# Optimization experiments

Hardware: AMD Instinct MI355X
Metric: run time of the kernel (lower is better)

## Reference

```python
import jax, jax.numpy as jnp
import numpy as np

B, S, IN_DIM = 8, 4096, 1024
N_SLOTS, SLOT_DIM, N_HEADS, CHUNK, TOP_K = 64, 256, 4, 16, 3
EPS_LN = 1e-5


def setup_inputs() -> dict:
    key = jax.random.key(0)
    ks = jax.random.split(key, 8)
    std = 0.02
    return {
        "x": jax.random.normal(ks[0], (B, S, IN_DIM), jnp.float32),
        "slot_memory": jax.random.normal(ks[1], (1, N_SLOTS, SLOT_DIM), jnp.float32) * std,
        "slot_keys": jax.random.normal(ks[2], (N_SLOTS, SLOT_DIM), jnp.float32) * std,
        "W_in": jax.random.normal(ks[3], (IN_DIM, SLOT_DIM), jnp.float32) / np.sqrt(IN_DIM).astype(np.float32),
        "W_write": jax.random.normal(ks[4], (SLOT_DIM, SLOT_DIM), jnp.float32) / np.sqrt(SLOT_DIM).astype(np.float32),
        "W_gate": jax.random.normal(ks[5], (2 * SLOT_DIM, 1), jnp.float32) / np.sqrt(2 * SLOT_DIM).astype(np.float32),
        "b_gate": jnp.zeros((1,), jnp.float32),
        "W_out": jax.random.normal(ks[6], (SLOT_DIM, IN_DIM), jnp.float32) / np.sqrt(SLOT_DIM).astype(np.float32),
        "ln_in_scale": jnp.ones((IN_DIM,), jnp.float32),
        "ln_in_bias": jnp.zeros((IN_DIM,), jnp.float32),
        "ln_s_scale": jnp.ones((SLOT_DIM,), jnp.float32),
        "ln_s_bias": jnp.zeros((SLOT_DIM,), jnp.float32),
    }


def _layer_norm(x, scale, bias):
    m = jnp.mean(x, axis=-1, keepdims=True)
    v = jnp.mean((x - m) ** 2, axis=-1, keepdims=True)
    return (x - m) * jax.lax.rsqrt(v + EPS_LN) * scale + bias


def _l2norm(x):
    n = jnp.sqrt(jnp.sum(x * x, axis=-1, keepdims=True))
    return x / jnp.maximum(n, 1e-12)  # matches F.normalize eps


def _forward(x, slot_memory, slot_keys, W_in, W_write, W_gate, b_gate, W_out,
             ln_in_scale, ln_in_bias, ln_s_scale, ln_s_bias):
    Bx, Sx, _ = x.shape
    hd = SLOT_DIM // N_HEADS
    slots0 = jnp.broadcast_to(slot_memory, (Bx, N_SLOTS, SLOT_DIM))

    # ---- batched read attention over slots ----
    q = _layer_norm(x, ln_in_scale, ln_in_bias) @ W_in          # (B,S,D)
    qh = q.reshape(Bx, Sx, N_HEADS, hd)
    kh = slots0.reshape(Bx, N_SLOTS, N_HEADS, hd)               # k == v == slots
    scores = jnp.einsum('bshd,bnhd->bhsn', qh, kh) * (hd ** -0.5)
    attn = jax.nn.softmax(scores, axis=-1)                      # (B,H,S,N)
    read = jnp.einsum('bhsn,bnhd->bshd', attn, kh).reshape(Bx, Sx, SLOT_DIM)

    # ---- sequential chunked top-k gather/scatter slot write ----
    key_norms = _l2norm(slot_keys)                              # (N,D)
    b_idx = jnp.arange(Bx)[:, None]

    def chunk_step(slots, chunk):                               # chunk: (B,C,D)
        summary = chunk.mean(axis=1)                            # (B,D)
        match = _l2norm(summary) @ key_norms.T                  # (B,N) cosine sim
        _, top_idx = jax.lax.top_k(match, TOP_K)                # (B,K)
        wv = summary @ W_write                                  # (B,D)
        sel = jnp.take_along_axis(slots, top_idx[:, :, None], axis=1)  # (B,K,D)
        gate = jax.nn.sigmoid(
            jnp.concatenate([sel.mean(axis=1), wv], axis=-1) @ W_gate + b_gate)  # (B,1)
        g = gate[:, None, :]
        new_vals = (1.0 - g) * sel + g * wv[:, None, :]         # (B,K,D)
        return slots.at[b_idx, top_idx].set(new_vals), None

    chunks = read.reshape(Bx, Sx // CHUNK, CHUNK, SLOT_DIM).transpose(1, 0, 2, 3)
    slots_f, _ = jax.lax.scan(chunk_step, slots0, chunks)
    new_slots = _layer_norm(slots_f, ln_s_scale, ln_s_bias)

    out = read @ W_out                                          # dropout is identity in eval
    return out, new_slots


def reference(x, slot_memory, slot_keys, W_in, W_write, W_gate, b_gate, W_out,
              ln_in_scale, ln_in_bias, ln_s_scale, ln_s_bias):
    return _forward(x, slot_memory, slot_keys, W_in, W_write, W_gate, b_gate, W_out,
                    ln_in_scale, ln_in_bias, ln_s_scale, ln_s_bias)
```

## Files before the change

kernel.cpp:

```cpp
#include <hip/hip_runtime.h>

typedef __attribute__((ext_vector_type(8))) short s8v;
typedef __attribute__((ext_vector_type(4))) float f4v;

#define PAD1 88
#define PADG 72

union U8 { unsigned u[4]; s8v s; };

__device__ __forceinline__ unsigned short f2bf(float f) {
  unsigned u = __float_as_uint(f);
  u += 0x7fffu + ((u >> 16) & 1u);
  return (unsigned short)(u >> 16);
}
__device__ __forceinline__ unsigned short f2bfc(float f) {
  return (unsigned short)((__float_as_uint(f) + 0x8000u) >> 16);
}
__device__ __forceinline__ float bf2f(unsigned short h) {
  return __uint_as_float(((unsigned)h) << 16);
}
__device__ __forceinline__ void split2(float x0, float x1, unsigned& hp, unsigned& lp) {
  unsigned t0 = __float_as_uint(x0) + 0x8000u;
  unsigned t1 = __float_as_uint(x1) + 0x8000u;
  float h0 = __uint_as_float(t0 & 0xFFFF0000u);
  float h1 = __uint_as_float(t1 & 0xFFFF0000u);
  float l0 = x0 - h0, l1 = x1 - h1;
  hp = __builtin_amdgcn_perm(t1, t0, 0x07060302u);
  lp = __builtin_amdgcn_perm(__float_as_uint(l1) + 0x8000u,
                             __float_as_uint(l0) + 0x8000u, 0x07060302u);
}
__device__ __forceinline__ unsigned pack2(float a, float b) {
  return __builtin_amdgcn_perm(__float_as_uint(b) + 0x8000u,
                               __float_as_uint(a) + 0x8000u, 0x07060302u);
}
__device__ __forceinline__ f4v vmax4(f4v a, f4v b) {
  f4v r; r[0]=fmaxf(a[0],b[0]); r[1]=fmaxf(a[1],b[1]); r[2]=fmaxf(a[2],b[2]); r[3]=fmaxf(a[3],b[3]); return r;
}
__device__ __forceinline__ f4v shflxor4(f4v v, int m) {
  f4v r; r[0]=__shfl_xor(v[0],m); r[1]=__shfl_xor(v[1],m); r[2]=__shfl_xor(v[2],m); r[3]=__shfl_xor(v[3],m); return r;
}
__device__ __forceinline__ f4v exp4(f4v v) {
  f4v r; r[0]=__expf(v[0]); r[1]=__expf(v[1]); r[2]=__expf(v[2]); r[3]=__expf(v[3]); return r;
}

__global__ void k_prep(const float* __restrict__ W_in, const float* __restrict__ lnis,
                       const float* __restrict__ lnib, const float* __restrict__ W_out,
                       const float* __restrict__ skeys, const float* __restrict__ smem0,
                       const float* __restrict__ wgate,
                       unsigned short* __restrict__ wth, unsigned short* __restrict__ wtl,
                       unsigned short* __restrict__ wot, float* __restrict__ keyn,
                       float* __restrict__ d0, float* __restrict__ uvec, float* __restrict__ vvec)
{
  __shared__ float pr[4];
  const int bid = blockIdx.x, tid = threadIdx.x;
  if (bid < 1024) {
    int idx = bid * 256 + tid;
    int n = idx >> 10, k = idx & 1023;
    float val = lnis[k] * W_in[k * 256 + n];
    unsigned short h = f2bf(val);
    wth[idx] = h;
    wtl[idx] = f2bf(val - bf2f(h));
  } else if (bid < 2048) {
    int idx = (bid - 1024) * 256 + tid;
    int n = idx >> 8, k = idx & 255;
    wot[idx] = f2bf(W_out[k * 1024 + n]);
  } else if (bid == 2048) {
    float su = 0.f, sv = 0.f;
    for (int i = 0; i < 1024; ++i) {
      float wv_ = W_in[i * 256 + tid];
      su += lnis[i] * wv_;
      sv += lnib[i] * wv_;
    }
    uvec[tid] = su; vvec[tid] = sv;
  } else {
    int n = bid - 2049;
    float sk = skeys[n * 256 + tid];
    float sq = sk * sk;
    #pragma unroll
    for (int m = 32; m; m >>= 1) sq += __shfl_xor(sq, m);
    if ((tid & 63) == 0) pr[tid >> 6] = sq;
    __syncthreads();
    float tot = pr[0] + pr[1] + pr[2] + pr[3];
    keyn[n * 256 + tid] = sk * (1.0f / fmaxf(sqrtf(tot), 1e-12f));
    float pd = smem0[n * 256 + tid] * wgate[tid];
    #pragma unroll
    for (int m = 32; m; m >>= 1) pd += __shfl_xor(pd, m);
    __syncthreads();
    if ((tid & 63) == 0) pr[tid >> 6] = pd;
    __syncthreads();
    if (tid == 0) d0[n] = pr[0] + pr[1] + pr[2] + pr[3];
  }
}

__global__ __launch_bounds__(512, 4) void k_gemm1(const float* __restrict__ x,
    const unsigned short* __restrict__ wth, const unsigned short* __restrict__ wtl,
    const float* __restrict__ uvec, const float* __restrict__ vvec,
    float* __restrict__ q)
{
  __shared__ unsigned short Ah[128 * PADG], Al[128 * PADG];
  __shared__ unsigned short Bh[128 * PADG], Bl[128 * PADG];
  __shared__ float uls[128], vls[128];
  __shared__ float mls[128], rls[128];
  const int tid = threadIdx.x;
  const int w = tid >> 6, lane = tid & 63;
  const int wm = w >> 2, wn = w & 3;
  const int mblk = blockIdx.x >> 1, nblk = blockIdx.x & 1;
  const int row0 = mblk * 128, n0 = nblk * 128;
  if (tid < 128) { uls[tid] = uvec[n0 + tid]; vls[tid] = vvec[n0 + tid]; }
  f4v zz = {0.f, 0.f, 0.f, 0.f};
  f4v acc[4][2];
  #pragma unroll
  for (int i = 0; i < 4; ++i)
    #pragma unroll
    for (int j = 0; j < 2; ++j) acc[i][j] = zz;
  const int rowA = tid >> 2, kqA = (tid & 3) * 16;
  float ps = 0.f, pss = 0.f;
  for (int kt = 0; kt < 16; ++kt) {
    const int k0 = kt * 64;
    {
      const float* src = x + (size_t)(row0 + rowA) * 1024 + k0 + kqA;
      float vv[16];
      #pragma unroll
      for (int i = 0; i < 4; ++i) *(f4v*)(vv + 4 * i) = *(const f4v*)(src + 4 * i);
      unsigned hp[8], lp[8];
      #pragma unroll
      for (int i = 0; i < 8; ++i) {
        ps += vv[2 * i] + vv[2 * i + 1];
        pss += vv[2 * i] * vv[2 * i] + vv[2 * i + 1] * vv[2 * i + 1];
        split2(vv[2 * i], vv[2 * i + 1], hp[i], lp[i]);
      }
      uint4* dh = (uint4*)&Ah[rowA * PADG + kqA];
      uint4* dl = (uint4*)&Al[rowA * PADG + kqA];
      dh[0] = make_uint4(hp[0], hp[1], hp[2], hp[3]);
      dh[1] = make_uint4(hp[4], hp[5], hp[6], hp[7]);
      dl[0] = make_uint4(lp[0], lp[1], lp[2], lp[3]);
      dl[1] = make_uint4(lp[4], lp[5], lp[6], lp[7]);
      const unsigned short* sh = wth + (size_t)(n0 + rowA) * 1024 + k0 + kqA;
      const unsigned short* sl = wtl + (size_t)(n0 + rowA) * 1024 + k0 + kqA;
      *(s8v*)&Bh[rowA * PADG + kqA] = *(const s8v*)sh;
      *(s8v*)&Bh[rowA * PADG + kqA + 8] = *(const s8v*)(sh + 8);
      *(s8v*)&Bl[rowA * PADG + kqA] = *(const s8v*)sl;
      *(s8v*)&Bl[rowA * PADG + kqA + 8] = *(const s8v*)(sl + 8);
    }
    __syncthreads();
    #pragma unroll
    for (int kk = 0; kk < 64; kk += 32) {
      const int kb = kk + (lane >> 4) * 8;
      s8v ah[4], al[4], bh[2], bl[2];
      #pragma unroll
      for (int mi = 0; mi < 4; ++mi) {
        const int rr = (wm * 64 + mi * 16 + (lane & 15)) * PADG + kb;
        ah[mi] = *(const s8v*)&Ah[rr];
        al[mi] = *(const s8v*)&Al[rr];
      }
      #pragma unroll
      for (int ni = 0; ni < 2; ++ni) {
        const int ccv = (wn * 32 + ni * 16 + (lane & 15)) * PADG + kb;
        bh[ni] = *(const s8v*)&Bh[ccv];
        bl[ni] = *(const s8v*)&Bl[ccv];
      }
      #pragma unroll
      for (int mi = 0; mi < 4; ++mi)
        #pragma unroll
        for (int ni = 0; ni < 2; ++ni) {
          acc[mi][ni] = __builtin_amdgcn_mfma_f32_16x16x32_bf16(ah[mi], bh[ni], acc[mi][ni], 0, 0, 0);
          acc[mi][ni] = __builtin_amdgcn_mfma_f32_16x16x32_bf16(ah[mi], bl[ni], acc[mi][ni], 0, 0, 0);
          acc[mi][ni] = __builtin_amdgcn_mfma_f32_16x16x32_bf16(al[mi], bh[ni], acc[mi][ni], 0, 0, 0);
        }
    }
    __syncthreads();
  }
  {
    float s0 = ps, s1 = pss;
    s0 += __shfl_xor(s0, 1); s1 += __shfl_xor(s1, 1);
    s0 += __shfl_xor(s0, 2); s1 += __shfl_xor(s1, 2);
    if ((tid & 3) == 0) {
      float mean = s0 * (1.0f / 1024.0f);
      mls[rowA] = mean;
      rls[rowA] = rsqrtf(s1 * (1.0f / 1024.0f) - mean * mean + 1e-5f);
    }
  }
  __syncthreads();
  #pragma unroll
  for (int mi = 0; mi < 4; ++mi)
    #pragma unroll
    for (int j = 0; j < 4; ++j) {
      const int lr = wm * 64 + mi * 16 + (lane >> 4) * 4 + j;
      const int r = row0 + lr;
      const float mv = mls[lr], rv = rls[lr];
      #pragma unroll
      for (int ni = 0; ni < 2; ++ni) {
        const int lc = wn * 32 + ni * 16 + (lane & 15);
        q[(size_t)r * 256 + n0 + lc] = rv * acc[mi][ni][j] - rv * mv * uls[lc] + vls[lc];
      }
    }
}

__global__ __launch_bounds__(512, 2) void k_attn(const float* __restrict__ q,
    const float* __restrict__ smem0, unsigned short* __restrict__ readb,
    float* __restrict__ summ)
{
  __shared__ float Kf[64 * 256];
  __shared__ float Pl[8][16 * 68];
  __shared__ float csm[8][64];
  const int tid = threadIdx.x;
  const int w = tid >> 6, lane = tid & 63;
  const int h = w & 3;
  const int l15 = lane & 15, kq = lane >> 4;

  {
    const int base = tid * 32;
    #pragma unroll
    for (int i = 0; i < 8; ++i)
      *(f4v*)&Kf[base + i * 4] = *(const f4v*)&smem0[base + i * 4];
  }
  __syncthreads();

  s8v bsh[4][2], bsl[4][2], bpv[4][2];
  #pragma unroll
  for (int nt = 0; nt < 4; ++nt)
    #pragma unroll
    for (int ks = 0; ks < 2; ++ks) {
      const float* src = &Kf[(nt * 16 + l15) * 256 + h * 64 + ks * 32 + kq * 8];
      float tmp[8];
      *(f4v*)tmp = *(const f4v*)src; *(f4v*)(tmp + 4) = *(const f4v*)(src + 4);
      U8 uh, ul;
      #pragma unroll
      for (int j = 0; j < 4; ++j) split2(tmp[2 * j], tmp[2 * j + 1], uh.u[j], ul.u[j]);
      bsh[nt][ks] = uh.s;
      bsl[nt][ks] = ul.s;
      U8 up;
      #pragma unroll
      for (int j = 0; j < 4; ++j)
        up.u[j] = pack2(Kf[(ks * 32 + kq * 8 + 2 * j) * 256 + h * 64 + nt * 16 + l15],
                        Kf[(ks * 32 + kq * 8 + 2 * j + 1) * 256 + h * 64 + nt * 16 + l15]);
      bpv[nt][ks] = up.s;
    }

  const int g0 = blockIdx.x * 8 + (w >> 2) * 4;
  f4v qv[2][4];
  {
    #pragma unroll
    for (int ks = 0; ks < 2; ++ks) {
      const float* qp = q + (size_t)(g0 * 16 + l15) * 256 + h * 64 + ks * 32 + kq * 8;
      qv[0][ks * 2] = *(const f4v*)qp;
      qv[0][ks * 2 + 1] = *(const f4v*)(qp + 4);
    }
  }
  #pragma unroll
  for (int i = 0; i < 4; ++i) {
    const int cur = i & 1, nxt = cur ^ 1;
    if (i < 3) {
      const int gn = g0 + i + 1;
      #pragma unroll
      for (int ks = 0; ks < 2; ++ks) {
        const float* qp = q + (size_t)(gn * 16 + l15) * 256 + h * 64 + ks * 32 + kq * 8;
        qv[nxt][ks * 2] = *(const f4v*)qp;
        qv[nxt][ks * 2 + 1] = *(const f4v*)(qp + 4);
      }
    }
    const int g = g0 + i;
    s8v ah[2], al[2];
    #pragma unroll
    for (int ks = 0; ks < 2; ++ks) {
      float tmp[8];
      *(f4v*)tmp = qv[cur][ks * 2]; *(f4v*)(tmp + 4) = qv[cur][ks * 2 + 1];
      U8 uh, ul;
      #pragma unroll
      for (int j = 0; j < 4; ++j) split2(tmp[2 * j], tmp[2 * j + 1], uh.u[j], ul.u[j]);
      ah[ks] = uh.s; al[ks] = ul.s;
    }
    f4v zz = {0.f, 0.f, 0.f, 0.f};
    f4v sacc[4] = {zz, zz, zz, zz};
    #pragma unroll
    for (int ks = 0; ks < 2; ++ks)
      #pragma unroll
      for (int nt = 0; nt < 4; ++nt) {
        sacc[nt] = __builtin_amdgcn_mfma_f32_16x16x32_bf16(ah[ks], bsh[nt][ks], sacc[nt], 0, 0, 0);
        sacc[nt] = __builtin_amdgcn_mfma_f32_16x16x32_bf16(ah[ks], bsl[nt][ks], sacc[nt], 0, 0, 0);
        sacc[nt] = __builtin_amdgcn_mfma_f32_16x16x32_bf16(al[ks], bsh[nt][ks], sacc[nt], 0, 0, 0);
      }
    #pragma unroll
    for (int nt = 0; nt < 4; ++nt) sacc[nt] = sacc[nt] * 0.125f;
    f4v mx = vmax4(vmax4(sacc[0], sacc[1]), vmax4(sacc[2], sacc[3]));
    #pragma unroll
    for (int m = 1; m <= 8; m <<= 1) mx = vmax4(mx, shflxor4(mx, m));
    f4v p[4];
    f4v psum = zz;
    #pragma unroll
    for (int nt = 0; nt < 4; ++nt) { p[nt] = exp4(sacc[nt] - mx); psum = psum + p[nt]; }
    #pragma unroll
    for (int m = 1; m <= 8; m <<= 1) psum = psum + shflxor4(psum, m);
    f4v rs;
    rs[0] = 1.0f / psum[0]; rs[1] = 1.0f / psum[1];
    rs[2] = 1.0f / psum[2]; rs[3] = 1.0f / psum[3];
    #pragma unroll
    for (int nt = 0; nt < 4; ++nt) p[nt] = p[nt] * rs;
    float cs4[4];
    #pragma unroll
    for (int nt = 0; nt < 4; ++nt) {
      cs4[nt] = p[nt][0] + p[nt][1] + p[nt][2] + p[nt][3];
      cs4[nt] += __shfl_xor(cs4[nt], 16);
      cs4[nt] += __shfl_xor(cs4[nt], 32);
    }
    if (kq == 0) {
      #pragma unroll
      for (int nt = 0; nt < 4; ++nt) csm[w][nt * 16 + l15] = cs4[nt];
    }
    #pragma unroll
    for (int nt = 0; nt < 4; ++nt)
      #pragma unroll
      for (int j = 0; j < 4; ++j)
        Pl[w][(kq * 4 + j) * 68 + nt * 16 + l15] = p[nt][j];
    s8v pa[2];
    #pragma unroll
    for (int ks = 0; ks < 2; ++ks) {
      const float* pp = &Pl[w][l15 * 68 + ks * 32 + kq * 8];
      float tmp[8];
      *(f4v*)tmp = *(const f4v*)pp; *(f4v*)(tmp + 4) = *(const f4v*)(pp + 4);
      U8 up;
      #pragma unroll
      for (int j = 0; j < 4; ++j) up.u[j] = pack2(tmp[2 * j], tmp[2 * j + 1]);
      pa[ks] = up.s;
    }
    f4v racc[4] = {zz, zz, zz, zz};
    #pragma unroll
    for (int ks = 0; ks < 2; ++ks)
      #pragma unroll
      for (int nt = 0; nt < 4; ++nt)
        racc[nt] = __builtin_amdgcn_mfma_f32_16x16x32_bf16(pa[ks], bpv[nt][ks], racc[nt], 0, 0, 0);
    const int rowbase = (g >> 8) * 4096 + (g & 255) * 16;
    #pragma unroll
    for (int nt = 0; nt < 4; ++nt)
      #pragma unroll
      for (int j = 0; j < 4; ++j)
        readb[(size_t)(rowbase + kq * 4 + j) * 256 + h * 64 + nt * 16 + l15] = f2bfc(racc[nt][j]);
    float s = 0.f;
    #pragma unroll 8
    for (int n = 0; n < 64; ++n) s += csm[w][n] * Kf[n * 256 + h * 64 + lane];
    summ[(size_t)g * 256 + h * 64 + lane] = s * (1.0f / 16.0f);
  }
}

__global__ void k_match(const float* __restrict__ summ, const float* __restrict__ keyn,
                        const float* __restrict__ Wwr, const float* __restrict__ wgate,
                        int* __restrict__ top3, float* __restrict__ wv,
                        float* __restrict__ wg2, float* __restrict__ dwv)
{
  __shared__ float sm[8][256];
  __shared__ float nrm_inv[8];
  __shared__ float mtch[8][64];
  __shared__ float redA[8][4], redB[8][4];
  const int tid = threadIdx.x, lane = tid & 63, w = tid >> 6;
  const int gbase = blockIdx.x * 8;
  #pragma unroll
  for (int gi = 0; gi < 8; ++gi) sm[gi][tid] = summ[(size_t)(gbase + gi) * 256 + tid];
  __syncthreads();
  {
    #pragma unroll
    for (int pass = 0; pass < 2; ++pass) {
      const int gi = w + pass * 4;
      float ss = 0.f;
      #pragma unroll
      for (int i = 0; i < 4; ++i) { float vv_ = sm[gi][lane + i * 64]; ss += vv_ * vv_; }
      #pragma unroll
      for (int m = 32; m; m >>= 1) ss += __shfl_xor(ss, m);
      if (lane == 0) nrm_inv[gi] = 1.0f / fmaxf(sqrtf(ss), 1e-12f);
    }
  }
  __syncthreads();
  {
    const int n = tid >> 2, qq = tid & 3;
    float mac[8] = {0.f, 0.f, 0.f, 0.f, 0.f, 0.f, 0.f, 0.f};
    const float* kp = keyn + n * 256 + qq * 64;
    for (int d = 0; d < 64; ++d) {
      float kv = kp[d];
      int dd = qq * 64 + d;
      #pragma unroll
      for (int gi = 0; gi < 8; ++gi) mac[gi] += sm[gi][dd] * kv;
    }
    #pragma unroll
    for (int gi = 0; gi < 8; ++gi) {
      float v2_ = mac[gi];
      v2_ += __shfl_xor(v2_, 1);
      v2_ += __shfl_xor(v2_, 2);
      if (qq == 0) mtch[gi][n] = v2_ * nrm_inv[gi];
    }
  }
  __syncthreads();
  {
    #pragma unroll
    for (int pass = 0; pass < 2; ++pass) {
      const int gi = w + pass * 4;
      float vorig = mtch[gi][lane];
      #pragma unroll
      for (int it = 0; it < 3; ++it) {
        float rv = vorig; int ri = lane;
        #pragma unroll
        for (int m = 32; m; m >>= 1) {
          float ov = __shfl_xor(rv, m); int oi = __shfl_xor(ri, m);
          if (ov > rv || (ov == rv && oi < ri)) { rv = ov; ri = oi; }
        }
        if (lane == 0) top3[(gbase + gi) * 4 + it] = ri;
        if (lane == ri) vorig = -3.0e38f;
      }
    }
  }
  float wva[8] = {0.f, 0.f, 0.f, 0.f, 0.f, 0.f, 0.f, 0.f};
  for (int d = 0; d < 256; ++d) {
    float ww = Wwr[(size_t)d * 256 + tid];
    #pragma unroll
    for (int gi = 0; gi < 8; ++gi) wva[gi] += sm[gi][d] * ww;
  }
  const float g1 = wgate[tid], g2 = wgate[256 + tid];
  #pragma unroll
  for (int gi = 0; gi < 8; ++gi) {
    wv[(size_t)(gbase + gi) * 256 + tid] = wva[gi];
    float p2 = wva[gi] * g2, p1 = wva[gi] * g1;
    #pragma unroll
    for (int m = 32; m; m >>= 1) { p2 += __shfl_xor(p2, m); p1 += __shfl_xor(p1, m); }
    if (lane == 0) { redA[gi][w] = p2; redB[gi][w] = p1; }
  }
  __syncthreads();
  if (tid < 8) {
    wg2[gbase + tid] = redA[tid][0] + redA[tid][1] + redA[tid][2] + redA[tid][3];
    dwv[gbase + tid] = redB[tid][0] + redB[tid][1] + redB[tid][2] + redB[tid][3];
  }
}

__global__ __launch_bounds__(1024) void k_scan(const float* __restrict__ d0,
    const int* __restrict__ top3, const float* __restrict__ wg2, const float* __restrict__ dwv,
    const float* __restrict__ bgate, const float* __restrict__ wv,
    const float* __restrict__ smem0, const float* __restrict__ lnss,
    const float* __restrict__ lnsb, float* __restrict__ outns)
{
  __shared__ float Wl[256][64];
  __shared__ float pn[64];
  __shared__ float wvs[32][256];
  __shared__ float gls[256];
  __shared__ int   pprm[256][4];
  __shared__ float dsl[64];
  const int bb = blockIdx.x, tid = threadIdx.x;
  const int lane = tid & 63;

  int ixA[4], iyA[4], izA[4];
  if (tid < 64) {
    const float bg = bgate[0];
    const float L2E = 1.4426950408889634f;
    #pragma unroll
    for (int j = 0; j < 4; ++j) {
      const int c = j * 64 + tid;
      int4 t3 = *(const int4*)&top3[(bb * 256 + c) * 4];
      ixA[j] = t3.x; iyA[j] = t3.y; izA[j] = t3.z;
      pprm[c][0] = t3.x | (t3.y << 6) | (t3.z << 12);
      pprm[c][1] = __float_as_int(-(wg2[bb * 256 + c] + bg) * L2E);
      pprm[c][2] = __float_as_int(dwv[bb * 256 + c]);
      pprm[c][3] = 0;
    }
    dsl[tid] = d0[tid];
  }
  __syncthreads();

  if (tid == 0) {
    const float COEFN = -0.48089834696298783f;
    #pragma unroll 2
    for (int c = 0; c < 256; ++c) {
      const int4 pr = *(const int4*)&pprm[c][0];
      const int i0 = pr.x & 63, i1 = (pr.x >> 6) & 63, i2 = (pr.x >> 12) & 63;
      const float wz = __int_as_float(pr.y);
      const float dv = __int_as_float(pr.z);
      const float a = dsl[i0], b = dsl[i1], d2 = dsl[i2];
      const float s3 = a + b + d2;
      const float e = __builtin_amdgcn_exp2f(fmaf(s3, COEFN, wz));
      const float g = __builtin_amdgcn_rcpf(1.0f + e);
      gls[c] = g;
      dsl[i0] = fmaf(g, dv - a, a);
      dsl[i1] = fmaf(g, dv - b, b);
      dsl[i2] = fmaf(g, dv - d2, d2);
    }
  }
  __syncthreads();

  if (tid < 64) {
    float running = 1.0f;
    #pragma unroll
    for (int j = 3; j >= 0; --j) {
      #pragma unroll 1
      for (int sl = 63; sl >= 0; --sl) {
        const int a0 = __builtin_amdgcn_readlane(ixA[j], sl);
        const int a1 = __builtin_amdgcn_readlane(iyA[j], sl);
        const int a2 = __builtin_amdgcn_readlane(izA[j], sl);
        const float gv = gls[j * 64 + sl];
        const bool hit = (lane == a0) | (lane == a1) | (lane == a2);
        Wl[j * 64 + sl][lane] = hit ? gv * running : 0.f;
        running = hit ? running * (1.0f - gv) : running;
      }
    }
    pn[lane] = running;
  }
  __syncthreads();

  const int n = tid >> 4, dq = tid & 15;
  float acc[16];
  {
    const float p = pn[n];
    const float* v0p = smem0 + n * 256 + dq * 16;
    #pragma unroll
    for (int i = 0; i < 16; i += 4) {
      f4v v0 = *(const f4v*)(v0p + i);
      acc[i] = p * v0[0]; acc[i + 1] = p * v0[1];
      acc[i + 2] = p * v0[2]; acc[i + 3] = p * v0[3];
    }
  }
  const int rr = tid >> 5, cc8 = (tid & 31) * 8;
  for (int ct = 0; ct < 8; ++ct) {
    __syncthreads();
    {
      const float* src = wv + (size_t)(bb * 256 + ct * 32 + rr) * 256 + cc8;
      *(f4v*)&wvs[rr][cc8] = *(const f4v*)src;
      *(f4v*)&wvs[rr][cc8 + 4] = *(const f4v*)(src + 4);
    }
    __syncthreads();
    #pragma unroll 1
    for (int cc = 0; cc < 32; ++cc) {
      const float coef = Wl[ct * 32 + cc][n];
      if (coef != 0.f) {
        const float* wp = &wvs[cc][dq * 16];
        #pragma unroll
        for (int i4 = 0; i4 < 4; ++i4) {
          f4v wq = *(const f4v*)(wp + i4 * 4);
          acc[i4 * 4 + 0] += coef * wq[0];
          acc[i4 * 4 + 1] += coef * wq[1];
          acc[i4 * 4 + 2] += coef * wq[2];
          acc[i4 * 4 + 3] += coef * wq[3];
        }
      }
    }
  }

  float s1 = 0.f;
  #pragma unroll
  for (int i = 0; i < 16; ++i) s1 += acc[i];
  #pragma unroll
  for (int m = 1; m < 16; m <<= 1) s1 += __shfl_xor(s1, m);
  const float mean = s1 * (1.0f / 256.0f);
  float s2 = 0.f;
  #pragma unroll
  for (int i = 0; i < 16; ++i) { float dd = acc[i] - mean; s2 += dd * dd; }
  #pragma unroll
  for (int m = 1; m < 16; m <<= 1) s2 += __shfl_xor(s2, m);
  const float rstd = rsqrtf(s2 * (1.0f / 256.0f) + 1e-5f);
  {
    const int base = (bb * 64 + n) * 256 + dq * 16;
    #pragma unroll
    for (int i = 0; i < 16; ++i) {
      int dd = dq * 16 + i;
      outns[base + i] = (acc[i] - mean) * rstd * lnss[dd] + lnsb[dd];
    }
  }
}

__global__ __launch_bounds__(512, 2) void k_gemm2(const unsigned short* __restrict__ a,
    const unsigned short* __restrict__ wot, float* __restrict__ out)
{
  __shared__ unsigned short As[128 * PAD1];
  __shared__ unsigned short Bs[256 * PAD1];
  const int tid = threadIdx.x;
  const int w = tid >> 6, lane = tid & 63;
  const int wm = w >> 2, wn = w & 3;
  const int mblk = blockIdx.x >> 2, nblk = blockIdx.x & 3;
  const int row0 = mblk * 128, n0 = nblk * 256;
  f4v zz = {0.f, 0.f, 0.f, 0.f};
  f4v acc[4][4];
  #pragma unroll
  for (int i = 0; i < 4; ++i)
    #pragma unroll
    for (int j = 0; j < 4; ++j) acc[i][j] = zz;
  const int rowA = tid >> 2, kqA = (tid & 3) * 16;
  const int colB = tid >> 1, khB = (tid & 1) * 32;
  for (int kt = 0; kt < 4; ++kt) {
    const int k0 = kt * 64;
    {
      const unsigned short* src = a + (size_t)(row0 + rowA) * 256 + k0 + kqA;
      *(s8v*)&As[rowA * PAD1 + kqA] = *(const s8v*)src;
      *(s8v*)&As[rowA * PAD1 + kqA + 8] = *(const s8v*)(src + 8);
      const unsigned short* sb = wot + (size_t)(n0 + colB) * 256 + k0 + khB;
      unsigned short* db = &Bs[colB * PAD1 + khB];
      #pragma unroll
      for (int i = 0; i < 4; ++i) *(s8v*)(db + 8 * i) = *(const s8v*)(sb + 8 * i);
    }
    __syncthreads();
    #pragma unroll
    for (int kk = 0; kk < 64; kk += 32) {
      const int kb = kk + (lane >> 4) * 8;
      s8v af[4], bf[4];
      #pragma unroll
      for (int mi = 0; mi < 4; ++mi)
        af[mi] = *(const s8v*)&As[(wm * 64 + mi * 16 + (lane & 15)) * PAD1 + kb];
      #pragma unroll
      for (int ni = 0; ni < 4; ++ni)
        bf[ni] = *(const s8v*)&Bs[(wn * 64 + ni * 16 + (lane & 15)) * PAD1 + kb];
      #pragma unroll
      for (int mi = 0; mi < 4; ++mi)
        #pragma unroll
        for (int ni = 0; ni < 4; ++ni)
          acc[mi][ni] = __builtin_amdgcn_mfma_f32_16x16x32_bf16(af[mi], bf[ni], acc[mi][ni], 0, 0, 0);
    }
    __syncthreads();
  }
  #pragma unroll
  for (int mi = 0; mi < 4; ++mi)
    #pragma unroll
    for (int j = 0; j < 4; ++j) {
      const int r = row0 + wm * 64 + mi * 16 + (lane >> 4) * 4 + j;
      #pragma unroll
      for (int ni = 0; ni < 4; ++ni) {
        const int cidx = wn * 64 + ni * 16 + (lane & 15);
        out[(size_t)r * 1024 + n0 + cidx] = acc[mi][ni][j];
      }
    }
}

extern "C" void kernel_launch(void* const* d_in, const int* in_sizes, int n_in,
                              void* d_out, int out_size, void* d_ws, size_t ws_size,
                              hipStream_t stream) {
  const float* x      = (const float*)d_in[0];
  const float* smem   = (const float*)d_in[1];
  const float* skeys  = (const float*)d_in[2];
  const float* W_in   = (const float*)d_in[3];
  const float* W_wr   = (const float*)d_in[4];
  const float* wgate  = (const float*)d_in[5];
  const float* bgate  = (const float*)d_in[6];
  const float* W_out  = (const float*)d_in[7];
  const float* lnis   = (const float*)d_in[8];
  const float* lnib   = (const float*)d_in[9];
  const float* lnss   = (const float*)d_in[10];
  const float* lnsb   = (const float*)d_in[11];
  (void)in_sizes; (void)n_in; (void)out_size; (void)ws_size;

  char* ws = (char*)d_ws;
  float*          q_buf = (float*)(ws + 0);
  unsigned short* readb = (unsigned short*)(ws + 134217728);
  float*          summ  = (float*)(ws + 150994944);
  float*          wv    = (float*)(ws + 153092096);
  unsigned short* wth   = (unsigned short*)(ws + 155189248);
  unsigned short* wtl   = (unsigned short*)(ws + 155713536);
  unsigned short* wot   = (unsigned short*)(ws + 156237824);
  float*          keyn  = (float*)(ws + 156762112);
  float*          uvec  = (float*)(ws + 157089792);
  float*          vvec  = (float*)(ws + 157090816);
  float*          d0    = (float*)(ws + 157091840);
  int*            top3  = (int*)(ws + 157092096);
  float*          wg2   = (float*)(ws + 157124864);
  float*          dwv   = (float*)(ws + 157133056);

  float* out   = (float*)d_out;
  float* outns = out + 33554432;

  k_prep<<<dim3(2113), dim3(256), 0, stream>>>(W_in, lnis, lnib, W_out, skeys, smem, wgate,
                                               wth, wtl, wot, keyn, d0, uvec, vvec);
  k_gemm1<<<dim3(512), dim3(512), 0, stream>>>(x, wth, wtl, uvec, vvec, q_buf);
  k_attn<<<dim3(256), dim3(512), 0, stream>>>(q_buf, smem, readb, summ);
  k_match<<<dim3(256), dim3(256), 0, stream>>>(summ, keyn, W_wr, wgate, top3, wv, wg2, dwv);
  k_scan<<<dim3(8), dim3(1024), 0, stream>>>(d0, top3, wg2, dwv, bgate, wv, smem, lnss, lnsb, outns);
  k_gemm2<<<dim3(1024), dim3(512), 0, stream>>>(readb, wot, out);
}
```

Before: 311.9 us.

## Load GEMM operand tiles directly into LDS with XOR-swizzled layout

Replaces register-staged global-to-shared copies of the bf16 weight tiles in gemm1 and of both operands in gemm2 with direct global_load_lds 16-byte transfers. The padded shared layouts become unpadded 64-wide rows with an XOR swizzle on the k offset to avoid bank conflicts. The aim is to cut VGPR traffic and load instructions and to shrink LDS use. Correctness depends on the async LDS loads being complete at the existing barrier, which relies on the compiler inserting the needed vmcnt waits.

Result: no change. 317.3 us (+1.8%).

```diff
diff --git a/kernel.cpp b/kernel.cpp
--- a/kernel.cpp
+++ b/kernel.cpp
@@ -3,10 +3,14 @@
 typedef __attribute__((ext_vector_type(8))) short s8v;
 typedef __attribute__((ext_vector_type(4))) float f4v;
 
-#define PAD1 88
 #define PADG 72
 
 union U8 { unsigned u[4]; s8v s; };
+
+__device__ __forceinline__ void gload16(const void* g, void* l) {
+  __builtin_amdgcn_global_load_lds((const __attribute__((address_space(1))) void*)g,
+                                   (__attribute__((address_space(3))) void*)l, 16, 0, 0);
+}
 
 __device__ __forceinline__ unsigned short f2bf(float f) {
   unsigned u = __float_as_uint(f);
@@ -98,7 +102,7 @@
     float* __restrict__ q)
 {
   __shared__ unsigned short Ah[128 * PADG], Al[128 * PADG];
-  __shared__ unsigned short Bh[128 * PADG], Bl[128 * PADG];
+  __shared__ unsigned short Bh[128 * 64], Bl[128 * 64];
   __shared__ float uls[128], vls[128];
   __shared__ float mls[128], rls[128];
   const int tid = threadIdx.x;
@@ -114,9 +118,16 @@
     #pragma unroll
     for (int j = 0; j < 2; ++j) acc[i][j] = zz;
   const int rowA = tid >> 2, kqA = (tid & 3) * 16;
+  const int grow = w * 8 + (lane >> 3);
+  const int gswz = ((lane & 7) ^ (lane >> 3)) << 3;
+  const size_t bsrc_h = (size_t)(n0 + grow) * 1024 + gswz;
   float ps = 0.f, pss = 0.f;
   for (int kt = 0; kt < 16; ++kt) {
     const int k0 = kt * 64;
+    gload16(wth + bsrc_h + k0,           &Bh[w * 512]);
+    gload16(wth + bsrc_h + 65536 + k0,   &Bh[4096 + w * 512]);
+    gload16(wtl + bsrc_h + k0,           &Bl[w * 512]);
+    gload16(wtl + bsrc_h + 65536 + k0,   &Bl[4096 + w * 512]);
     {
       const float* src = x + (size_t)(row0 + rowA) * 1024 + k0 + kqA;
       float vv[16];
@@ -135,12 +146,6 @@
       dh[1] = make_uint4(hp[4], hp[5], hp[6], hp[7]);
       dl[0] = make_uint4(lp[0], lp[1], lp[2], lp[3]);
       dl[1] = make_uint4(lp[4], lp[5], lp[6], lp[7]);
-      const unsigned short* sh = wth + (size_t)(n0 + rowA) * 1024 + k0 + kqA;
-      const unsigned short* sl = wtl + (size_t)(n0 + rowA) * 1024 + k0 + kqA;
-      *(s8v*)&Bh[rowA * PADG + kqA] = *(const s8v*)sh;
-      *(s8v*)&Bh[rowA * PADG + kqA + 8] = *(const s8v*)(sh + 8);
-      *(s8v*)&Bl[rowA * PADG + kqA] = *(const s8v*)sl;
-      *(s8v*)&Bl[rowA * PADG + kqA + 8] = *(const s8v*)(sl + 8);
     }
     __syncthreads();
     #pragma unroll
@@ -155,7 +160,8 @@
       }
       #pragma unroll
       for (int ni = 0; ni < 2; ++ni) {
-        const int ccv = (wn * 32 + ni * 16 + (lane & 15)) * PADG + kb;
+        const int r = wn * 32 + ni * 16 + (lane & 15);
+        const int ccv = r * 64 + (kb ^ ((r & 7) * 8));
         bh[ni] = *(const s8v*)&Bh[ccv];
         bl[ni] = *(const s8v*)&Bl[ccv];
       }
@@ -563,8 +569,8 @@
 __global__ __launch_bounds__(512, 2) void k_gemm2(const unsigned short* __restrict__ a,
     const unsigned short* __restrict__ wot, float* __restrict__ out)
 {
-  __shared__ unsigned short As[128 * PAD1];
-  __shared__ unsigned short Bs[256 * PAD1];
+  __shared__ unsigned short As[128 * 64];
+  __shared__ unsigned short Bs[256 * 64];
   const int tid = threadIdx.x;
   const int w = tid >> 6, lane = tid & 63;
   const int wm = w >> 2, wn = w & 3;
@@ -576,30 +582,30 @@
   for (int i = 0; i < 4; ++i)
     #pragma unroll
     for (int j = 0; j < 4; ++j) acc[i][j] = zz;
-  const int rowA = tid >> 2, kqA = (tid & 3) * 16;
-  const int colB = tid >> 1, khB = (tid & 1) * 32;
+  const int grow = w * 8 + (lane >> 3);
+  const int gswz = ((lane & 7) ^ (lane >> 3)) << 3;
   for (int kt = 0; kt < 4; ++kt) {
     const int k0 = kt * 64;
-    {
-      const unsigned short* src = a + (size_t)(row0 + rowA) * 256 + k0 + kqA;
-      *(s8v*)&As[rowA * PAD1 + kqA] = *(const s8v*)src;
-      *(s8v*)&As[rowA * PAD1 + kqA + 8] = *(const s8v*)(src + 8);
-      const unsigned short* sb = wot + (size_t)(n0 + colB) * 256 + k0 + khB;
-      unsigned short* db = &Bs[colB * PAD1 + khB];
-      #pragma unroll
-      for (int i = 0; i < 4; ++i) *(s8v*)(db + 8 * i) = *(const s8v*)(sb + 8 * i);
-    }
+    gload16(a + (size_t)(row0 + grow) * 256 + k0 + gswz,        &As[w * 512]);
+    gload16(a + (size_t)(row0 + 64 + grow) * 256 + k0 + gswz,   &As[4096 + w * 512]);
+    #pragma unroll
+    for (int i = 0; i < 4; ++i)
+      gload16(wot + (size_t)(n0 + i * 64 + grow) * 256 + k0 + gswz, &Bs[i * 4096 + w * 512]);
     __syncthreads();
     #pragma unroll
     for (int kk = 0; kk < 64; kk += 32) {
       const int kb = kk + (lane >> 4) * 8;
       s8v af[4], bf[4];
       #pragma unroll
-      for (int mi = 0; mi < 4; ++mi)
-        af[mi] = *(const s8v*)&As[(wm * 64 + mi * 16 + (lane & 15)) * PAD1 + kb];
-      #pragma unroll
-      for (int ni = 0; ni < 4; ++ni)
-        bf[ni] = *(const s8v*)&Bs[(wn * 64 + ni * 16 + (lane & 15)) * PAD1 + kb];
+      for (int mi = 0; mi < 4; ++mi) {
+        const int r = wm * 64 + mi * 16 + (lane & 15);
+        af[mi] = *(const s8v*)&As[r * 64 + (kb ^ ((r & 7) * 8))];
+      }
+      #pragma unroll
+      for (int ni = 0; ni < 4; ++ni) {
+        const int r = wn * 64 + ni * 16 + (lane & 15);
+        bf[ni] = *(const s8v*)&Bs[r * 64 + (kb ^ ((r & 7) * 8))];
+      }
       #pragma unroll
       for (int mi = 0; mi < 4; ++mi)
         #pragma unroll
```
